# Kernel tuning notes

Hardware: AMD Instinct MI355X
Metric: run time of the kernel (lower is better)

The kernel has to match this reference:

```python
import jax, jax.numpy as jnp
import numpy as np

NFFT = 4194304          # FFT size / number of subcarriers
SPACING = 16            # pilot spacing
P = NFFT // SPACING     # num_pilots = 262144


def setup_inputs() -> dict:
    key = jax.random.key(0)
    k1, k2, k3, k4 = jax.random.split(key, 4)
    Y_real = jax.random.normal(k1, (NFFT,), dtype=jnp.float32)
    Y_imag = jax.random.normal(k2, (NFFT,), dtype=jnp.float32)
    # pilot symbols kept away from zero so the complex division is well-conditioned
    Xp_real = jax.random.normal(k3, (P,), dtype=jnp.float32) + 2.0
    Xp_imag = jax.random.normal(k4, (P,), dtype=jnp.float32)
    weights = jnp.ones((P,), dtype=jnp.float32)          # estimation_weights param
    alpha = jnp.float32(0.5)                             # interp_alpha param
    beta = jnp.float32(0.5)                              # interp_beta param
    gamma = jnp.float32(0.0)                             # interp_gamma param
    # evenly spaced 0-based pilot positions: 0, 16, ..., NFFT-16 (sorted, unique)
    pilot_pos = jnp.arange(P, dtype=jnp.int32) * SPACING
    return {"Y_real": Y_real, "Y_imag": Y_imag, "Xp_real": Xp_real,
            "Xp_imag": Xp_imag, "weights": weights, "alpha": alpha,
            "beta": beta, "gamma": gamma, "pilot_pos": pilot_pos, "Nfft": NFFT}


def reference(Y_real, Y_imag, Xp_real, Xp_imag, weights, alpha, beta, gamma,
              pilot_pos, Nfft):
    # ---- per-pilot LS estimate: LS[k] = Y[pilot_pos[k]] / Xp[k] (complex div) ----
    Yr = Y_real[pilot_pos]
    Yi = Y_imag[pilot_pos]
    den = Xp_real * Xp_real + Xp_imag * Xp_imag
    LSr = (Yr * Xp_real + Yi * Xp_imag) / den
    LSi = (Yi * Xp_real - Yr * Xp_imag) / den
    # weighted LS (estimation_weights[:len(pilot_pos)] == weights)
    Hr = LSr * weights
    Hi = LSi * weights

    # ---- pilot_loc handling (torch passes 1-based; min==1 -> subtract back) ----
    loc = pilot_pos.astype(jnp.float32)  # (pilot_pos + 1) - 1
    # first pilot is at 0 -> no front extension.
    # last pilot (Nfft - SPACING) < Nfft - 1 -> linear-extrapolate one endpoint.
    dx = loc[-1] - loc[-2]
    slope_r = (Hr[-1] - Hr[-2]) / dx
    slope_i = (Hi[-1] - Hi[-2]) / dx
    d_end = jnp.float32(Nfft - 1) - loc[-1]
    Hr = jnp.concatenate([Hr, Hr[-1:] + slope_r * d_end])
    Hi = jnp.concatenate([Hi, Hi[-1:] + slope_i * d_end])
    loc = jnp.concatenate([loc, jnp.array([Nfft - 1], dtype=jnp.float32)])

    # ---- trainable interpolation, vectorized over all Nfft subcarriers ----
    idx = jnp.arange(Nfft, dtype=jnp.float32)
    left = jnp.clip(jnp.searchsorted(loc, idx, side='right') - 1,
                    0, loc.shape[0] - 2)
    right = left + 1
    X0 = loc[left]
    X1 = loc[right]
    df = jnp.where(X1 - X0 > 0, (idx - X0) / (X1 - X0), 0.0)
    # out = alpha * H[right] + beta * H[left] + gamma * df
    # (gamma * df is real -> it only affects the real part, as in torch complex add)
    out_r = alpha * Hr[right] + beta * Hr[left] + gamma * df
    out_i = alpha * Hi[right] + beta * Hi[left]
    return jnp.stack([out_r, out_i], axis=-1)  # [Nfft, 2] = (real, imag)
```

## Files before the change

### kernel.cpp

```cpp
#include <hip/hip_runtime.h>


typedef float f32x4 __attribute__((ext_vector_type(4)));

constexpr int NT      = 128;
constexpr int PAIRS   = 8;
constexpr int CHUNK   = NT * PAIRS * 2;
constexpr int SPACING = 16;

__global__ __launch_bounds__(NT) void ce_kernel(
    const float* __restrict__ Y_real, const float* __restrict__ Y_imag,
    const float* __restrict__ Xp_real, const float* __restrict__ Xp_imag,
    const float* __restrict__ weights,
    const float* __restrict__ alpha_p, const float* __restrict__ beta_p,
    const float* __restrict__ gamma_p,
    f32x4* __restrict__ out4, int Nfft, int P)
{
    constexpr int NP = CHUNK / SPACING;
    __shared__ float sHr [NP + 1];
    __shared__ float sHi [NP + 1];

    const int t    = threadIdx.x;
    const int p0   = blockIdx.x * NP;
    const int base = blockIdx.x * CHUNK;

    const float a = *alpha_p;
    const float b = *beta_p;
    const float g = *gamma_p;

    auto ls = [&](int kk, float& hr, float& hi) {
        float yr = Y_real[(size_t)kk * SPACING], yi = Y_imag[(size_t)kk * SPACING];
        float xr = Xp_real[kk],                  xi = Xp_imag[kk];
        float inv = 1.0f / (xr * xr + xi * xi);
        float wk  = weights[kk];
        hr = (yr * xr + yi * xi) * inv * wk;
        hi = (yi * xr - yr * xi) * inv * wk;
    };

    {
        const int k = p0 + t;
        float hr, hi; ls(k, hr, hi);
        sHr[t] = hr; sHi[t] = hi;
    }
    if (t == 0) {
        int ke = p0 + NP;
        if (ke < P) {
            float hr, hi; ls(ke, hr, hi);
            sHr[NP] = hr; sHi[NP] = hi;
        } else {
            float hr1, hi1, hr2, hi2;
            ls(P - 1, hr1, hi1);
            ls(P - 2, hr2, hi2);
            float l1 = (float)((P - 1) * SPACING);
            float l2 = (float)((P - 2) * SPACING);
            float inv_dx = 1.0f / (l1 - l2);
            float dend   = (float)(Nfft - 1) - l1;
            sHr[NP] = hr1 + (hr1 - hr2) * inv_dx * dend;
            sHi[NP] = hi1 + (hi1 - hi2) * inv_dx * dend;
        }
    }
    __syncthreads();

    const bool lastBlock = (p0 + NP >= P);

    #pragma unroll
    for (int j = 0; j < PAIRS; ++j) {
        int i0 = base + j * (NT * 2) + 2 * t;
        int lp = (i0 >> 4) - p0;
        float inv = (lastBlock && lp == NP - 1)
                        ? (1.0f / (float)(SPACING - 1))
                        : (1.0f / (float)SPACING);
        float X0  = (float)((p0 + lp) * SPACING);
        float df0 = ((float)i0 - X0) * inv;
        float hr0 = sHr[lp], hr1 = sHr[lp + 1];
        float hi0 = sHi[lp], hi1 = sHi[lp + 1];
        float rr = a * hr1 + b * hr0;
        float ii = a * hi1 + b * hi0;
        f32x4 o;
        o.x = rr + g * df0;
        o.y = ii;
        o.z = rr + g * (df0 + inv);
        o.w = ii;
        __builtin_nontemporal_store(o, &out4[(base >> 1) + j * NT + t]);
    }
}

extern "C" void kernel_launch(void* const* d_in, const int* in_sizes, int n_in,
                              void* d_out, int out_size, void* d_ws, size_t ws_size,
                              hipStream_t stream) {
    const float* Yr = (const float*)d_in[0];
    const float* Yi = (const float*)d_in[1];
    const float* Xr = (const float*)d_in[2];
    const float* Xi = (const float*)d_in[3];
    const float* w  = (const float*)d_in[4];
    const float* al = (const float*)d_in[5];
    const float* be = (const float*)d_in[6];
    const float* ga = (const float*)d_in[7];
    const int Nfft = in_sizes[0];
    const int P    = in_sizes[2];

    const int grid = (Nfft + CHUNK - 1) / CHUNK;
    ce_kernel<<<grid, NT, 0, stream>>>(Yr, Yi, Xr, Xi, w, al, be, ga,
                                       (f32x4*)d_out, Nfft, P);
}
```

Baseline: 14.86 us.

## Split pilot LS estimation into a separate kernel writing to workspace

```diff
diff --git a/kernel.cpp b/kernel.cpp
--- a/kernel.cpp
+++ b/kernel.cpp
@@ -7,11 +7,42 @@
 constexpr int PAIRS   = 8;
 constexpr int CHUNK   = NT * PAIRS * 2;
 constexpr int SPACING = 16;
+constexpr int NTA     = 256;
 
-__global__ __launch_bounds__(NT) void ce_kernel(
+__global__ __launch_bounds__(NTA) void pilot_kernel(
     const float* __restrict__ Y_real, const float* __restrict__ Y_imag,
     const float* __restrict__ Xp_real, const float* __restrict__ Xp_imag,
     const float* __restrict__ weights,
+    float* __restrict__ Hr, float* __restrict__ Hi, int Nfft, int P)
+{
+    const int k = blockIdx.x * NTA + threadIdx.x;
+    if (k >= P) return;
+
+    auto ls = [&](int kk, float& hr, float& hi) {
+        float yr = Y_real[(size_t)kk * SPACING], yi = Y_imag[(size_t)kk * SPACING];
+        float xr = Xp_real[kk],                  xi = Xp_imag[kk];
+        float inv = 1.0f / (xr * xr + xi * xi);
+        float wk  = weights[kk];
+        hr = (yr * xr + yi * xi) * inv * wk;
+        hi = (yi * xr - yr * xi) * inv * wk;
+    };
+
+    float hr, hi; ls(k, hr, hi);
+    Hr[k] = hr; Hi[k] = hi;
+
+    if (k == P - 1) {
+        float hr2, hi2; ls(P - 2, hr2, hi2);
+        float l1 = (float)((P - 1) * SPACING);
+        float l2 = (float)((P - 2) * SPACING);
+        float inv_dx = 1.0f / (l1 - l2);
+        float dend   = (float)(Nfft - 1) - l1;
+        Hr[P] = hr + (hr - hr2) * inv_dx * dend;
+        Hi[P] = hi + (hi - hi2) * inv_dx * dend;
+    }
+}
+
+__global__ __launch_bounds__(NT) void interp_kernel(
+    const float* __restrict__ Hr, const float* __restrict__ Hi,
     const float* __restrict__ alpha_p, const float* __restrict__ beta_p,
     const float* __restrict__ gamma_p,
     f32x4* __restrict__ out4, int Nfft, int P)
@@ -28,36 +59,11 @@
     const float b = *beta_p;
     const float g = *gamma_p;
 
-    auto ls = [&](int kk, float& hr, float& hi) {
-        float yr = Y_real[(size_t)kk * SPACING], yi = Y_imag[(size_t)kk * SPACING];
-        float xr = Xp_real[kk],                  xi = Xp_imag[kk];
-        float inv = 1.0f / (xr * xr + xi * xi);
-        float wk  = weights[kk];
-        hr = (yr * xr + yi * xi) * inv * wk;
-        hi = (yi * xr - yr * xi) * inv * wk;
-    };
-
-    {
-        const int k = p0 + t;
-        float hr, hi; ls(k, hr, hi);
-        sHr[t] = hr; sHi[t] = hi;
-    }
+    sHr[t] = Hr[p0 + t];
+    sHi[t] = Hi[p0 + t];
     if (t == 0) {
-        int ke = p0 + NP;
-        if (ke < P) {
-            float hr, hi; ls(ke, hr, hi);
-            sHr[NP] = hr; sHi[NP] = hi;
-        } else {
-            float hr1, hi1, hr2, hi2;
-            ls(P - 1, hr1, hi1);
-            ls(P - 2, hr2, hi2);
-            float l1 = (float)((P - 1) * SPACING);
-            float l2 = (float)((P - 2) * SPACING);
-            float inv_dx = 1.0f / (l1 - l2);
-            float dend   = (float)(Nfft - 1) - l1;
-            sHr[NP] = hr1 + (hr1 - hr2) * inv_dx * dend;
-            sHi[NP] = hi1 + (hi1 - hi2) * inv_dx * dend;
-        }
+        sHr[NP] = Hr[p0 + NP];
+        sHi[NP] = Hi[p0 + NP];
     }
     __syncthreads();
 
@@ -99,7 +105,13 @@
     const int Nfft = in_sizes[0];
     const int P    = in_sizes[2];
 
+    float* Hr = (float*)d_ws;
+    float* Hi = Hr + (P + 1);
+
+    pilot_kernel<<<(P + NTA - 1) / NTA, NTA, 0, stream>>>(
+        Yr, Yi, Xr, Xi, w, Hr, Hi, Nfft, P);
+
     const int grid = (Nfft + CHUNK - 1) / CHUNK;
-    ce_kernel<<<grid, NT, 0, stream>>>(Yr, Yi, Xr, Xi, w, al, be, ga,
-                                       (f32x4*)d_out, Nfft, P);
+    interp_kernel<<<grid, NT, 0, stream>>>(
+        Hr, Hi, al, be, ga, (f32x4*)d_out, Nfft, P);
 }
```

Measured after the change: 18.46 us. +24.3%, slower.
